# Optimization experiments

Measured on AMD Instinct MI355X. Metric: run time of the kernel, lower is better.

Reference implementation:

```python
import jax, jax.numpy as jnp
import numpy as np
import math

B = 16          # graphs per batch
N = 2048        # nodes per graph
F_IN = 64       # input node features
E_PER = 32768   # edges per graph
E = B * E_PER
H = 128         # hidden width (fixed by module)
C = 10          # output classes
K = math.ceil(0.8 * N)  # TopKPooling keep count per graph = 1639


def setup_inputs() -> dict:
    key = jax.random.key(0)
    ks = jax.random.split(key, 24)
    x = jax.random.normal(ks[0], (B * N, F_IN), jnp.float32)
    # intra-graph random edges (source->target), global node ids
    gid = jnp.repeat(jnp.arange(B, dtype=jnp.int32), E_PER)
    src = gid * N + jax.random.randint(ks[1], (E,), 0, N, dtype=jnp.int32)
    dst = gid * N + jax.random.randint(ks[2], (E,), 0, N, dtype=jnp.int32)

    def lin_w(k, o, i):
        return jax.random.normal(k, (o, i), jnp.float32) / jnp.sqrt(i)

    inp = dict(x=x, src=src, dst=dst)
    # GraphConv: lin_rel (with bias) on aggregated neighbors + lin_root (no bias)
    inp.update(W1_rel=lin_w(ks[3], H, F_IN), b1=jnp.zeros((H,), jnp.float32), W1_root=lin_w(ks[4], H, F_IN))
    inp.update(W2_rel=lin_w(ks[5], H, H), b2=jnp.zeros((H,), jnp.float32), W2_root=lin_w(ks[6], H, H))
    inp.update(W3_rel=lin_w(ks[7], H, H), b3=jnp.zeros((H,), jnp.float32), W3_root=lin_w(ks[8], H, H))
    inp.update(pool_w=jax.random.normal(ks[9], (H,), jnp.float32) / jnp.sqrt(H))
    inp.update(Wl1=lin_w(ks[10], 128, 256), bl1=jnp.zeros((128,), jnp.float32))
    inp.update(Wl2=lin_w(ks[11], 64, 128), bl2=jnp.zeros((64,), jnp.float32))
    inp.update(Wl3=lin_w(ks[12], C, 64), bl3=jnp.zeros((C,), jnp.float32))
    return inp


def _graph_conv(x, src, dst, W_rel, b, W_root, n_nodes, emask=None):
    # out_i = W_rel @ (sum_{j->i} x_j) + b + W_root @ x_i
    msg = x[src]
    if emask is not None:
        msg = msg * emask[:, None]
    agg = jax.ops.segment_sum(msg, dst, num_segments=n_nodes)
    return agg @ W_rel.T + b + x @ W_root.T


def _global_pools(x, n_per_graph):
    xb = x.reshape(B, n_per_graph, -1)
    return jnp.concatenate([xb.max(axis=1), xb.mean(axis=1)], axis=1)  # [B, 2F]


def reference(x, src, dst, W1_rel, b1, W1_root, W2_rel, b2, W2_root,
              W3_rel, b3, W3_root, pool_w, Wl1, bl1, Wl2, bl2, Wl3, bl3):
    n0 = B * N
    h = jax.nn.relu(_graph_conv(x, src, dst, W1_rel, b1, W1_root, n0))
    x1 = _global_pools(h, N)

    h = jax.nn.relu(_graph_conv(h, src, dst, W2_rel, b2, W2_root, n0))

    # TopKPooling(ratio=0.8): score = tanh(x@w/||w||); keep top-k per graph;
    # kept features scaled by score; edges with a dropped endpoint removed.
    score = jnp.tanh((h @ pool_w) / jnp.linalg.norm(pool_w))  # [B*N]
    top_s, top_i = jax.lax.top_k(score.reshape(B, N), K)      # [B,K]
    perm = (top_i + jnp.arange(B)[:, None] * N).reshape(-1)   # global old ids [B*K]
    h = h[perm] * top_s.reshape(-1)[:, None]                  # [B*K, H]

    n1 = B * K
    new_id = jnp.full((n0,), -1, jnp.int32).at[perm].set(jnp.arange(n1, dtype=jnp.int32))
    ns, nd = new_id[src], new_id[dst]
    keep = ((ns >= 0) & (nd >= 0)).astype(h.dtype)
    ns = jnp.where(ns >= 0, ns, 0)
    nd = jnp.where(nd >= 0, nd, 0)

    x2 = _global_pools(h, K)
    h = jax.nn.relu(_graph_conv(h, ns, nd, W3_rel, b3, W3_root, n1, emask=keep))
    x3 = _global_pools(h, K)

    z = x1 + x2 + x3
    z = jax.nn.relu(z @ Wl1.T + bl1)
    z = jax.nn.relu(z @ Wl2.T + bl2)
    return jax.nn.log_softmax(z @ Wl3.T + bl3, axis=-1)  # [B, C]
```

## Files before the change

### kernel.cpp

```cpp
#include <hip/hip_runtime.h>
#include <hip/hip_bf16.h>
#include <math.h>

#define NB 32768
#define NN 2048
#define BG 16
#define KK 1639
#define KKP 1664
#define N1 (BG*KK)
#define N1P (BG*KKP)
#define EE 524288
#define HH 128
#define FIN 64

using half8 = __attribute__((ext_vector_type(8))) _Float16;
using half4 = __attribute__((ext_vector_type(4))) _Float16;
using f32x4 = __attribute__((ext_vector_type(4))) float;

__device__ __forceinline__ void acc4(f32x4& a, const float4& v) {
  a[0] += v.x; a[1] += v.y; a[2] += v.z; a[3] += v.w;
}

__global__ void deg_kernel(const int* __restrict__ dst, int* deg, int n) {
  int e = blockIdx.x * blockDim.x + threadIdx.x;
  if (e < n) atomicAdd(&deg[dst[e]], 1);
}

__global__ void exscan_kernel(const int* __restrict__ deg, int* rs, int* cursor, int n) {
  __shared__ int wsum[16];
  __shared__ int carry;
  int t = threadIdx.x;
  int lane = t & 63, wid = t >> 6;
  if (t == 0) carry = 0;
  __syncthreads();
  int ntiles = (n + 4095) >> 12;
  for (int tile = 0; tile < ntiles; ++tile) {
    int idx = (tile << 12) + t * 4;
    int4 v4 = *(const int4*)(deg + idx);
    int v0 = (idx + 0 < n) ? v4.x : 0;
    int v1 = (idx + 1 < n) ? v4.y : 0;
    int v2 = (idx + 2 < n) ? v4.z : 0;
    int v3 = (idx + 3 < n) ? v4.w : 0;
    int s = v0 + v1 + v2 + v3;
    int pre = s;
#pragma unroll
    for (int off = 1; off < 64; off <<= 1) {
      int u = __shfl_up(pre, off, 64);
      if (lane >= off) pre += u;
    }
    if (lane == 63) wsum[wid] = pre;
    __syncthreads();
    int wbase = 0;
#pragma unroll
    for (int ww = 0; ww < 16; ++ww)
      if (ww < wid) wbase += wsum[ww];
    int ex = carry + wbase + (pre - s);
    int4 e4 = make_int4(ex, ex + v0, ex + v0 + v1, ex + v0 + v1 + v2);
    if (idx + 3 < n) {
      *(int4*)(rs + idx) = e4;
      *(int4*)(cursor + idx) = e4;
    } else {
      if (idx + 0 < n) { rs[idx + 0] = e4.x; cursor[idx + 0] = e4.x; }
      if (idx + 1 < n) { rs[idx + 1] = e4.y; cursor[idx + 1] = e4.y; }
      if (idx + 2 < n) { rs[idx + 2] = e4.z; cursor[idx + 2] = e4.z; }
    }
    int tot = 0;
    if (t == 1023) tot = ex + s;
    __syncthreads();
    if (t == 1023) carry = tot;
    __syncthreads();
  }
  if (t == 0) rs[n] = carry;
}

__global__ void scatter_kernel(const int* __restrict__ src, const int* __restrict__ dst,
                               int* cursor, int* csr, int n) {
  int e = blockIdx.x * blockDim.x + threadIdx.x;
  if (e < n) {
    int d = dst[e];
    int p = atomicAdd(&cursor[d], 1);
    csr[p] = src[e];
  }
}

template <int KD1, int KD2, int POOL, int SCORE, int REMAP>
__global__ __launch_bounds__(512, 4) void conv_mfma(
    const float* __restrict__ feat, const float* __restrict__ xr,
    const int* __restrict__ rs, const int* __restrict__ csr,
    const int* __restrict__ perm, const int* __restrict__ new_id,
    const _Float16* __restrict__ Wh, const _Float16* __restrict__ Wl,
    const float* __restrict__ bias, float* __restrict__ out, int M, int nwg,
    float* __restrict__ pmax, float* __restrict__ psum,
    const float* __restrict__ pw, float* __restrict__ score) {
  constexpr int KTOT = KD1 + KD2;
  constexpr int NSTEP = KTOT / 32;
  __shared__ _Float16 ah_lds[64 * KTOT];
  __shared__ _Float16 al_lds[64 * KTOT];
  __shared__ float sdot[64][8];
  __shared__ float swsq[8];

  int tid = threadIdx.x;
  int lane = tid & 63, wid = tid >> 6;
  int bq = nwg >> 3, br = nwg & 7, bx = blockIdx.x & 7, bi = blockIdx.x >> 3;
  int swz = (bx < br ? bx * (bq + 1) : br * (bq + 1) + (bx - br) * bq) + bi;
  int row0 = swz * 64;
  int ch0 = wid * 16;
  int col = lane & 15;
  int kseg = (lane >> 4) * 8;

  {
    constexpr int CH = KD1 / 4;
    constexpr int EPW = 64 / CH;
    int sub = lane / CH;
    int ch = lane % CH;
    const float4* feat4 = (const float4*)feat;
#pragma unroll
    for (int rr = 0; rr < 8; ++rr) {
      int gr = wid * 8 + rr;
      int grow = row0 + gr;
      int e0 = 0, e1 = 0;
      if (REMAP) {
        int g = grow / KKP, j = grow - g * KKP;
        if (j < KK) {
          int oldrow = perm[g * KK + j];
          e0 = rs[oldrow];
          e1 = rs[oldrow + 1];
        }
      } else {
        if (grow >= M) grow = M - 1;
        e0 = rs[grow];
        e1 = rs[grow + 1];
      }
      f32x4 a0 = {0.f, 0.f, 0.f, 0.f}, a1 = a0, a2 = a0, a3 = a0;
      int e = e0 + sub;
      for (; e + 7 * EPW < e1; e += 8 * EPW) {
        int c[8];
#pragma unroll
        for (int u = 0; u < 8; ++u) c[u] = csr[e + u * EPW];
        if (REMAP) {
#pragma unroll
          for (int u = 0; u < 8; ++u) c[u] = new_id[c[u]];
        }
        float4 v[8];
#pragma unroll
        for (int u = 0; u < 8; ++u) {
          int ci = (REMAP && c[u] < 0) ? 0 : c[u];
          v[u] = feat4[(size_t)ci * CH + ch];
        }
        if (REMAP) {
#pragma unroll
          for (int u = 0; u < 8; ++u)
            if (c[u] < 0) v[u] = make_float4(0.f, 0.f, 0.f, 0.f);
        }
        acc4(a0, v[0]); acc4(a1, v[1]); acc4(a2, v[2]); acc4(a3, v[3]);
        acc4(a0, v[4]); acc4(a1, v[5]); acc4(a2, v[6]); acc4(a3, v[7]);
      }
      for (; e + 3 * EPW < e1; e += 4 * EPW) {
        int c[4];
#pragma unroll
        for (int u = 0; u < 4; ++u) c[u] = csr[e + u * EPW];
        if (REMAP) {
#pragma unroll
          for (int u = 0; u < 4; ++u) c[u] = new_id[c[u]];
        }
        float4 v[4];
#pragma unroll
        for (int u = 0; u < 4; ++u) {
          int ci = (REMAP && c[u] < 0) ? 0 : c[u];
          v[u] = feat4[(size_t)ci * CH + ch];
        }
        if (REMAP) {
#pragma unroll
          for (int u = 0; u < 4; ++u)
            if (c[u] < 0) v[u] = make_float4(0.f, 0.f, 0.f, 0.f);
        }
        acc4(a0, v[0]); acc4(a1, v[1]); acc4(a2, v[2]); acc4(a3, v[3]);
      }
      for (; e < e1; e += EPW) {
        int c = csr[e];
        if (REMAP) {
          c = new_id[c];
          if (c < 0) continue;
        }
        float4 v = feat4[(size_t)c * CH + ch];
        acc4(a0, v);
      }
      f32x4 s = (a0 + a1) + (a2 + a3);
      if (EPW == 4) {
#pragma unroll
        for (int j = 0; j < 4; ++j) s[j] += __shfl_xor(s[j], 16, 64);
      }
#pragma unroll
      for (int j = 0; j < 4; ++j) s[j] += __shfl_xor(s[j], 32, 64);
      if (sub == 0) {
        half4 hi, lo;
#pragma unroll
        for (int j = 0; j < 4; ++j) {
          _Float16 h = (_Float16)s[j];
          hi[j] = h;
          lo[j] = (_Float16)(s[j] - (float)h);
        }
        int byte = ((gr * KTOT + ch * 4) * 2) ^ ((gr & 7) << 4);
        *(half4*)((char*)ah_lds + byte) = hi;
        *(half4*)((char*)al_lds + byte) = lo;
      }
    }
  }

  for (int idx = tid; idx < 64 * KD2 / 8; idx += 512) {
    int row = idx / (KD2 / 8);
    int kc = (idx % (KD2 / 8)) * 8;
    int grow = row0 + row;
    if (grow >= M) grow = M - 1;
    const float* sp = xr + (size_t)grow * KD2 + kc;
    float4 a0 = *(const float4*)sp;
    float4 a1 = *(const float4*)(sp + 4);
    float av[8] = {a0.x, a0.y, a0.z, a0.w, a1.x, a1.y, a1.z, a1.w};
    half8 vh, vl;
#pragma unroll
    for (int j = 0; j < 8; ++j) {
      _Float16 h = (_Float16)av[j];
      vh[j] = h;
      vl[j] = (_Float16)(av[j] - (float)h);
    }
    int byte = ((row * KTOT + KD1 + kc) * 2) ^ ((row & 7) << 4);
    *(half8*)((char*)ah_lds + byte) = vh;
    *(half8*)((char*)al_lds + byte) = vl;
  }

  size_t wbase = (size_t)(ch0 + col) * KTOT + kseg;
  half8 whc = *(const half8*)(Wh + wbase);
  half8 wlc = *(const half8*)(Wl + wbase);
  __syncthreads();

  f32x4 acc[4];
#pragma unroll
  for (int rf = 0; rf < 4; ++rf) acc[rf] = (f32x4){0.f, 0.f, 0.f, 0.f};
  int r = lane & 15;
#pragma unroll
  for (int s = 0; s < NSTEP; ++s) {
    half8 whn, wln;
    if (s + 1 < NSTEP) {
      whn = *(const half8*)(Wh + wbase + (s + 1) * 32);
      wln = *(const half8*)(Wl + wbase + (s + 1) * 32);
    }
#pragma unroll
    for (int rf = 0; rf < 4; ++rf) {
      int row = rf * 16 + r;
      int byte = ((row * KTOT + s * 32 + kseg) * 2) ^ ((row & 7) << 4);
      half8 a_h = *(const half8*)((const char*)ah_lds + byte);
      half8 a_l = *(const half8*)((const char*)al_lds + byte);
      acc[rf] = __builtin_amdgcn_mfma_f32_16x16x32_f16(a_l, whc, acc[rf], 0, 0, 0);
      acc[rf] = __builtin_amdgcn_mfma_f32_16x16x32_f16(a_h, wlc, acc[rf], 0, 0, 0);
      acc[rf] = __builtin_amdgcn_mfma_f32_16x16x32_f16(a_h, whc, acc[rf], 0, 0, 0);
    }
    if (s + 1 < NSTEP) { whc = whn; wlc = wln; }
  }

  float bv = bias[ch0 + col];
  float cmax = -3.402823466e38f, csum = 0.f;
  float wcol = SCORE ? pw[ch0 + col] : 0.f;
  float pd[4][4];
  int g = 0, rowbase = 0;
  if (POOL == 2) { g = row0 / KKP; rowbase = row0 - g * KKP; }
#pragma unroll
  for (int rf = 0; rf < 4; ++rf) {
    int orow0 = row0 + rf * 16 + (lane >> 4) * 4;
#pragma unroll
    for (int rr = 0; rr < 4; ++rr) {
      int orow = orow0 + rr;
      float v = fmaxf(acc[rf][rr] + bv, 0.f);
      if (orow < M) out[(size_t)orow * HH + ch0 + col] = v;
      if (POOL == 1) { cmax = fmaxf(cmax, v); csum += v; }
      if (POOL == 2) {
        int local = rowbase + rf * 16 + (lane >> 4) * 4 + rr;
        if (local < KK) { cmax = fmaxf(cmax, v); csum += v; }
      }
      if (SCORE) pd[rf][rr] = v * wcol;
    }
  }
  if (POOL) {
    cmax = fmaxf(cmax, __shfl_xor(cmax, 16, 64)); csum += __shfl_xor(csum, 16, 64);
    cmax = fmaxf(cmax, __shfl_xor(cmax, 32, 64)); csum += __shfl_xor(csum, 32, 64);
    if ((lane >> 4) == 0) {
      if (POOL == 1) {
        int gg = row0 >> 11, sb = (row0 & 2047) >> 6;
        pmax[(gg * 32 + sb) * HH + ch0 + col] = cmax;
        psum[(gg * 32 + sb) * HH + ch0 + col] = csum;
      } else {
        int sb = rowbase >> 6;
        pmax[(g * 26 + sb) * HH + ch0 + col] = cmax;
        psum[(g * 26 + sb) * HH + ch0 + col] = csum;
      }
    }
  }
  if (SCORE) {
#pragma unroll
    for (int rf = 0; rf < 4; ++rf)
#pragma unroll
      for (int rr = 0; rr < 4; ++rr) {
        float d = pd[rf][rr];
        d += __shfl_xor(d, 1, 64); d += __shfl_xor(d, 2, 64);
        d += __shfl_xor(d, 4, 64); d += __shfl_xor(d, 8, 64);
        if (col == 0) sdot[rf * 16 + (lane >> 4) * 4 + rr][wid] = d;
      }
    float wsq = wcol * wcol;
    wsq += __shfl_xor(wsq, 1, 64); wsq += __shfl_xor(wsq, 2, 64);
    wsq += __shfl_xor(wsq, 4, 64); wsq += __shfl_xor(wsq, 8, 64);
    if (lane == 0) swsq[wid] = wsq;
    __syncthreads();
    if (tid < 64) {
      float d = 0.f, q = 0.f;
#pragma unroll
      for (int wv = 0; wv < 8; ++wv) { d += sdot[tid][wv]; q += swsq[wv]; }
      score[row0 + tid] = tanhf(d * rsqrtf(q));
    }
  }
}

__global__ void prep_weights_f16(const float* __restrict__ W1_rel, const float* __restrict__ W1_root,
                                 const float* __restrict__ W2_rel, const float* __restrict__ W2_root,
                                 const float* __restrict__ W3_rel, const float* __restrict__ W3_root,
                                 _Float16* wh1, _Float16* wl1, _Float16* wh2, _Float16* wl2,
                                 _Float16* wh3, _Float16* wl3) {
  int idx = blockIdx.x * blockDim.x + threadIdx.x;
  float v;
  _Float16* ph;
  _Float16* pl;
  int j;
  if (idx < 128 * 128) {
    j = idx;
    int o = j >> 7, k = j & 127;
    v = (k < 64) ? W1_rel[o * 64 + k] : W1_root[o * 64 + (k - 64)];
    ph = wh1; pl = wl1;
  } else if (idx < 128 * 128 + 128 * 256) {
    j = idx - 128 * 128;
    int o = j >> 8, k = j & 255;
    v = (k < 128) ? W2_rel[o * 128 + k] : W2_root[o * 128 + (k - 128)];
    ph = wh2; pl = wl2;
  } else if (idx < 128 * 128 + 2 * 128 * 256) {
    j = idx - 128 * 128 - 128 * 256;
    int o = j >> 8, k = j & 255;
    v = (k < 128) ? W3_rel[o * 128 + k] : W3_root[o * 128 + (k - 128)];
    ph = wh3; pl = wl3;
  } else {
    return;
  }
  _Float16 h = (_Float16)v;
  ph[j] = h;
  pl[j] = (_Float16)(v - (float)h);
}

__global__ void topk_kernel(const float* __restrict__ score, int* perm) {
  __shared__ unsigned long long keys[NN];
  __shared__ int hist[256];
  __shared__ unsigned long long sP;
  __shared__ int srem;
  __shared__ int scnt;
  int b = blockIdx.x, t = threadIdx.x;
  for (int i = t; i < NN; i += 256) {
    float s = score[b * NN + i];
    unsigned u = __float_as_uint(s);
    u = (u & 0x80000000u) ? ~u : (u | 0x80000000u);
    keys[i] = ((unsigned long long)u << 32) | (unsigned)(NN - 1 - i);
  }
  if (t == 0) { sP = 0ULL; srem = KK; scnt = 0; }
  __syncthreads();
  for (int pass = 0; pass < 8; ++pass) {
    int shift = 56 - 8 * pass;
    for (int i = t; i < 256; i += 256) hist[i] = 0;
    __syncthreads();
    unsigned long long P = sP;
    unsigned long long hm = (pass == 0) ? 0ULL : (~0ULL) << (shift + 8);
    for (int i = t; i < NN; i += 256) {
      unsigned long long k = keys[i];
      if (((k ^ P) & hm) == 0) atomicAdd(&hist[(int)((k >> shift) & 255)], 1);
    }
    __syncthreads();
    if (t < 64) {
      int l = t;
      int c[4], part = 0;
#pragma unroll
      for (int q = 0; q < 4; ++q) { c[q] = hist[255 - (l * 4 + q)]; part += c[q]; }
      int pre = part;
#pragma unroll
      for (int off = 1; off < 64; off <<= 1) {
        int u2 = __shfl_up(pre, off, 64);
        if (l >= off) pre += u2;
      }
      int excl = pre - part;
      int rem = srem;
      if (excl < rem && rem <= excl + part) {
        int run = excl;
#pragma unroll
        for (int q = 0; q < 4; ++q) {
          if (run + c[q] >= rem) {
            srem = rem - run;
            sP = sP | ((unsigned long long)(255 - (l * 4 + q)) << shift);
            break;
          }
          run += c[q];
        }
      }
    }
    __syncthreads();
  }
  unsigned long long T = sP;
  for (int i = t; i < NN; i += 256) {
    if (keys[i] >= T) {
      int pos = atomicAdd(&scnt, 1);
      perm[b * KK + pos] = b * NN + (NN - 1 - (int)(keys[i] & 0xffffffffULL));
    }
  }
}

__global__ void h3_kernel(const float4* __restrict__ h2, const int* __restrict__ perm,
                          const float* __restrict__ score, float4* __restrict__ h3,
                          int* __restrict__ new_id) {
  int idx = blockIdx.x * blockDim.x + threadIdx.x;
  if (idx < N1 * 32) {
    int g = idx >> 5, c = idx & 31;
    int b = g / KK, j = g - b * KK;
    int p = perm[g];
    if (c == 0) new_id[p] = b * KKP + j;
    float s = score[p];
    float4 v = h2[(size_t)p * 32 + c];
    v.x *= s; v.y *= s; v.z *= s; v.w *= s;
    h3[(size_t)(b * KKP + j) * 32 + c] = v;
  }
}

__global__ void pool2_kernel(const float* __restrict__ h, float* pmax, float* psum) {
  int b = blockIdx.x / 26, s = blockIdx.x % 26;
  int f = threadIdx.x;
  int r0 = s * 64, r1 = min(KK, r0 + 64);
  float m = -3.402823466e38f, sum = 0.f;
  for (int r = r0; r < r1; ++r) {
    float v = h[(size_t)(b * KKP + r) * HH + f];
    m = fmaxf(m, v);
    sum += v;
  }
  pmax[(b * 26 + s) * HH + f] = m;
  psum[(b * 26 + s) * HH + f] = sum;
}

__global__ void mlp_kernel(const float* __restrict__ pm1, const float* __restrict__ ps1,
                           const float* __restrict__ pm2, const float* __restrict__ ps2,
                           const float* __restrict__ pm3, const float* __restrict__ ps3,
                           const float* __restrict__ Wl1, const float* __restrict__ bl1,
                           const float* __restrict__ Wl2, const float* __restrict__ bl2,
                           const float* __restrict__ Wl3, const float* __restrict__ bl3,
                           float* out) {
  __shared__ float z[256], a1[128], a2[64], a3[10], red[2];
  int b = blockIdx.x, t = threadIdx.x;
  float m1 = -3.402823466e38f, m2 = m1, m3 = m1;
  float s1 = 0.f, s2 = 0.f, s3 = 0.f;
  for (int s = 0; s < 32; ++s) {
    int o = (b * 32 + s) * 128 + t;
    m1 = fmaxf(m1, pm1[o]); s1 += ps1[o];
  }
  for (int s = 0; s < 26; ++s) {
    int o = (b * 26 + s) * 128 + t;
    m2 = fmaxf(m2, pm2[o]); s2 += ps2[o];
    m3 = fmaxf(m3, pm3[o]); s3 += ps3[o];
  }
  z[t] = m1 + m2 + m3;
  z[128 + t] = s1 * (1.f / NN) + (s2 + s3) * (1.f / KK);
  __syncthreads();
  {
    float acc = bl1[t];
    for (int q = 0; q < 256; ++q) acc = fmaf(Wl1[t * 256 + q], z[q], acc);
    a1[t] = fmaxf(acc, 0.f);
  }
  __syncthreads();
  if (t < 64) {
    float acc = bl2[t];
    for (int q = 0; q < 128; ++q) acc = fmaf(Wl2[t * 128 + q], a1[q], acc);
    a2[t] = fmaxf(acc, 0.f);
  }
  __syncthreads();
  if (t < 10) {
    float acc = bl3[t];
    for (int q = 0; q < 64; ++q) acc = fmaf(Wl3[t * 64 + q], a2[q], acc);
    a3[t] = acc;
  }
  __syncthreads();
  if (t == 0) {
    float m = a3[0];
    for (int i = 1; i < 10; ++i) m = fmaxf(m, a3[i]);
    float s = 0.f;
    for (int i = 0; i < 10; ++i) s += expf(a3[i] - m);
    red[0] = m;
    red[1] = logf(s);
  }
  __syncthreads();
  if (t < 10) out[b * 10 + t] = a3[t] - red[0] - red[1];
}

extern "C" void kernel_launch(void* const* d_in, const int* in_sizes, int n_in,
                              void* d_out, int out_size, void* d_ws, size_t ws_size,
                              hipStream_t stream) {
  const float* x       = (const float*)d_in[0];
  const int*   src     = (const int*)d_in[1];
  const int*   dst     = (const int*)d_in[2];
  const float* W1_rel  = (const float*)d_in[3];
  const float* b1      = (const float*)d_in[4];
  const float* W1_root = (const float*)d_in[5];
  const float* W2_rel  = (const float*)d_in[6];
  const float* b2      = (const float*)d_in[7];
  const float* W2_root = (const float*)d_in[8];
  const float* W3_rel  = (const float*)d_in[9];
  const float* b3      = (const float*)d_in[10];
  const float* W3_root = (const float*)d_in[11];
  const float* pool_w  = (const float*)d_in[12];
  const float* Wl1     = (const float*)d_in[13];
  const float* bl1     = (const float*)d_in[14];
  const float* Wl2     = (const float*)d_in[15];
  const float* bl2     = (const float*)d_in[16];
  const float* Wl3     = (const float*)d_in[17];
  const float* bl3     = (const float*)d_in[18];
  float* out = (float*)d_out;

  char* w = (char*)d_ws;
  size_t off = 0;
  auto alloc = [&](size_t bytes) -> char* {
    off = (off + 255) & ~(size_t)255;
    char* p = w + off;
    off += bytes;
    return p;
  };
  int* deg1     = (int*)alloc((NB + 4096) * 4);
  int* rs1      = (int*)alloc((NB + 1) * 4);
  int* cursor1  = (int*)alloc(NB * 4);
  int* csr1     = (int*)alloc((size_t)EE * 4);
  int* new_id   = (int*)alloc(NB * 4);
  int* perm     = (int*)alloc(N1 * 4);
  _Float16* wh1 = (_Float16*)alloc(128 * 128 * 2);
  _Float16* wl1 = (_Float16*)alloc(128 * 128 * 2);
  _Float16* wh2 = (_Float16*)alloc(128 * 256 * 2);
  _Float16* wl2 = (_Float16*)alloc(128 * 256 * 2);
  _Float16* wh3 = (_Float16*)alloc(128 * 256 * 2);
  _Float16* wl3 = (_Float16*)alloc(128 * 256 * 2);
  float* bufA   = (float*)alloc((size_t)NB * HH * 4);
  float* bufB   = (float*)alloc((size_t)NB * HH * 4);
  float* score  = (float*)alloc(NB * 4);
  float* pm1    = (float*)alloc(BG * 32 * HH * 4);
  float* ps1    = (float*)alloc(BG * 32 * HH * 4);
  float* pm2    = (float*)alloc(BG * 26 * HH * 4);
  float* ps2    = (float*)alloc(BG * 26 * HH * 4);
  float* pm3    = (float*)alloc(BG * 26 * HH * 4);
  float* ps3    = (float*)alloc(BG * 26 * HH * 4);
  if (off > ws_size) return;

  const int TB = 256;
  const int egrid = (EE + TB - 1) / TB;

  hipMemsetAsync(deg1, 0, (NB + 4096) * 4, stream);
  hipMemsetAsync(new_id, 0xFF, NB * 4, stream);

  prep_weights_f16<<<(128 * 128 + 2 * 128 * 256 + TB - 1) / TB, TB, 0, stream>>>(
      W1_rel, W1_root, W2_rel, W2_root, W3_rel, W3_root, wh1, wl1, wh2, wl2, wh3, wl3);

  deg_kernel<<<egrid, TB, 0, stream>>>(dst, deg1, EE);
  exscan_kernel<<<1, 1024, 0, stream>>>(deg1, rs1, cursor1, NB);
  scatter_kernel<<<egrid, TB, 0, stream>>>(src, dst, cursor1, csr1, EE);

  conv_mfma<64, 64, 1, 0, 0><<<NB / 64, 512, 0, stream>>>(
      x, x, rs1, csr1, nullptr, nullptr, wh1, wl1, b1, bufA, NB, NB / 64, pm1, ps1,
      nullptr, nullptr);

  conv_mfma<128, 128, 0, 1, 0><<<NB / 64, 512, 0, stream>>>(
      bufA, bufA, rs1, csr1, nullptr, nullptr, wh2, wl2, b2, bufB, NB, NB / 64,
      nullptr, nullptr, pool_w, score);

  topk_kernel<<<BG, 256, 0, stream>>>(score, perm);
  h3_kernel<<<(N1 * 32 + TB - 1) / TB, TB, 0, stream>>>((const float4*)bufB, perm, score,
                                                        (float4*)bufA, new_id);
  pool2_kernel<<<BG * 26, 128, 0, stream>>>(bufA, pm2, ps2);

  conv_mfma<128, 128, 2, 0, 1><<<N1P / 64, 512, 0, stream>>>(
      bufA, bufA, rs1, csr1, perm, new_id, wh3, wl3, b3, bufB, N1P, N1P / 64, pm3, ps3,
      nullptr, nullptr);

  mlp_kernel<<<BG, 128, 0, stream>>>(pm1, ps1, pm2, ps2, pm3, ps3,
                                     Wl1, bl1, Wl2, bl2, Wl3, bl3, out);
}
```

Baseline: 227.5 us.

## Precompute remapped CSR and row ranges for pooled conv; fold memsets into prep

Adds a remap pass that writes a new-id-translated copy of the CSR column array, and has h3_kernel record per-new-row edge start/end offsets. The third conv then reads those directly instead of doing a dependent new_id lookup per edge and a perm/rs indirection per row. The two hipMemsetAsync calls are folded into the weight-prep kernel. This costs an extra full pass over the edge list and extra workspace for csr3.

```diff
diff --git a/kernel.cpp b/kernel.cpp
--- a/kernel.cpp
+++ b/kernel.cpp
@@ -83,11 +83,17 @@
   }
 }
 
+__global__ void remap_kernel(const int* __restrict__ csr1, const int* __restrict__ new_id,
+                             int* __restrict__ csr3, int n) {
+  int e = blockIdx.x * blockDim.x + threadIdx.x;
+  if (e < n) csr3[e] = new_id[csr1[e]];
+}
+
 template <int KD1, int KD2, int POOL, int SCORE, int REMAP>
 __global__ __launch_bounds__(512, 4) void conv_mfma(
     const float* __restrict__ feat, const float* __restrict__ xr,
     const int* __restrict__ rs, const int* __restrict__ csr,
-    const int* __restrict__ perm, const int* __restrict__ new_id,
+    const int* __restrict__ rows3, const int* __restrict__ rowe3,
     const _Float16* __restrict__ Wh, const _Float16* __restrict__ Wl,
     const float* __restrict__ bias, float* __restrict__ out, int M, int nwg,
     float* __restrict__ pmax, float* __restrict__ psum,
@@ -118,14 +124,10 @@
     for (int rr = 0; rr < 8; ++rr) {
       int gr = wid * 8 + rr;
       int grow = row0 + gr;
-      int e0 = 0, e1 = 0;
+      int e0, e1;
       if (REMAP) {
-        int g = grow / KKP, j = grow - g * KKP;
-        if (j < KK) {
-          int oldrow = perm[g * KK + j];
-          e0 = rs[oldrow];
-          e1 = rs[oldrow + 1];
-        }
+        e0 = rows3[grow];
+        e1 = rowe3[grow];
       } else {
         if (grow >= M) grow = M - 1;
         e0 = rs[grow];
@@ -137,10 +139,6 @@
         int c[8];
 #pragma unroll
         for (int u = 0; u < 8; ++u) c[u] = csr[e + u * EPW];
-        if (REMAP) {
-#pragma unroll
-          for (int u = 0; u < 8; ++u) c[u] = new_id[c[u]];
-        }
         float4 v[8];
 #pragma unroll
         for (int u = 0; u < 8; ++u) {
@@ -159,10 +157,6 @@
         int c[4];
 #pragma unroll
         for (int u = 0; u < 4; ++u) c[u] = csr[e + u * EPW];
-        if (REMAP) {
-#pragma unroll
-          for (int u = 0; u < 4; ++u) c[u] = new_id[c[u]];
-        }
         float4 v[4];
 #pragma unroll
         for (int u = 0; u < 4; ++u) {
@@ -178,10 +172,7 @@
       }
       for (; e < e1; e += EPW) {
         int c = csr[e];
-        if (REMAP) {
-          c = new_id[c];
-          if (c < 0) continue;
-        }
+        if (REMAP && c < 0) continue;
         float4 v = feat4[(size_t)c * CH + ch];
         acc4(a0, v);
       }
@@ -318,12 +309,17 @@
   }
 }
 
-__global__ void prep_weights_f16(const float* __restrict__ W1_rel, const float* __restrict__ W1_root,
-                                 const float* __restrict__ W2_rel, const float* __restrict__ W2_root,
-                                 const float* __restrict__ W3_rel, const float* __restrict__ W3_root,
-                                 _Float16* wh1, _Float16* wl1, _Float16* wh2, _Float16* wl2,
-                                 _Float16* wh3, _Float16* wl3) {
+__global__ void prep_kernel(const float* __restrict__ W1_rel, const float* __restrict__ W1_root,
+                            const float* __restrict__ W2_rel, const float* __restrict__ W2_root,
+                            const float* __restrict__ W3_rel, const float* __restrict__ W3_root,
+                            _Float16* wh1, _Float16* wl1, _Float16* wh2, _Float16* wl2,
+                            _Float16* wh3, _Float16* wl3,
+                            int* __restrict__ deg1, int* __restrict__ new_id,
+                            int* __restrict__ rows3, int* __restrict__ rowe3) {
   int idx = blockIdx.x * blockDim.x + threadIdx.x;
+  if (idx < NB + 4096) deg1[idx] = 0;
+  if (idx < NB) new_id[idx] = -1;
+  if (idx < N1P) { rows3[idx] = 0; rowe3[idx] = 0; }
   float v;
   _Float16* ph;
   _Float16* pl;
@@ -415,18 +411,24 @@
 }
 
 __global__ void h3_kernel(const float4* __restrict__ h2, const int* __restrict__ perm,
-                          const float* __restrict__ score, float4* __restrict__ h3,
-                          int* __restrict__ new_id) {
+                          const float* __restrict__ score, const int* __restrict__ rs1,
+                          float4* __restrict__ h3, int* __restrict__ new_id,
+                          int* __restrict__ rows3, int* __restrict__ rowe3) {
   int idx = blockIdx.x * blockDim.x + threadIdx.x;
   if (idx < N1 * 32) {
     int g = idx >> 5, c = idx & 31;
     int b = g / KK, j = g - b * KK;
     int p = perm[g];
-    if (c == 0) new_id[p] = b * KKP + j;
+    int pj = b * KKP + j;
+    if (c == 0) {
+      new_id[p] = pj;
+      rows3[pj] = rs1[p];
+      rowe3[pj] = rs1[p + 1];
+    }
     float s = score[p];
     float4 v = h2[(size_t)p * 32 + c];
     v.x *= s; v.y *= s; v.z *= s; v.w *= s;
-    h3[(size_t)(b * KKP + j) * 32 + c] = v;
+    h3[(size_t)pj * 32 + c] = v;
   }
 }
 
@@ -533,8 +535,11 @@
   int* rs1      = (int*)alloc((NB + 1) * 4);
   int* cursor1  = (int*)alloc(NB * 4);
   int* csr1     = (int*)alloc((size_t)EE * 4);
+  int* csr3     = (int*)alloc((size_t)EE * 4);
   int* new_id   = (int*)alloc(NB * 4);
   int* perm     = (int*)alloc(N1 * 4);
+  int* rows3    = (int*)alloc(N1P * 4);
+  int* rowe3    = (int*)alloc(N1P * 4);
   _Float16* wh1 = (_Float16*)alloc(128 * 128 * 2);
   _Float16* wl1 = (_Float16*)alloc(128 * 128 * 2);
   _Float16* wh2 = (_Float16*)alloc(128 * 256 * 2);
@@ -555,11 +560,9 @@
   const int TB = 256;
   const int egrid = (EE + TB - 1) / TB;
 
-  hipMemsetAsync(deg1, 0, (NB + 4096) * 4, stream);
-  hipMemsetAsync(new_id, 0xFF, NB * 4, stream);
-
-  prep_weights_f16<<<(128 * 128 + 2 * 128 * 256 + TB - 1) / TB, TB, 0, stream>>>(
-      W1_rel, W1_root, W2_rel, W2_root, W3_rel, W3_root, wh1, wl1, wh2, wl2, wh3, wl3);
+  prep_kernel<<<(128 * 128 + 2 * 128 * 256 + TB - 1) / TB, TB, 0, stream>>>(
+      W1_rel, W1_root, W2_rel, W2_root, W3_rel, W3_root, wh1, wl1, wh2, wl2, wh3, wl3,
+      deg1, new_id, rows3, rowe3);
 
   deg_kernel<<<egrid, TB, 0, stream>>>(dst, deg1, EE);
   exscan_kernel<<<1, 1024, 0, stream>>>(deg1, rs1, cursor1, NB);
@@ -575,11 +578,13 @@
 
   topk_kernel<<<BG, 256, 0, stream>>>(score, perm);
   h3_kernel<<<(N1 * 32 + TB - 1) / TB, TB, 0, stream>>>((const float4*)bufB, perm, score,
-                                                        (float4*)bufA, new_id);
+                                                        rs1, (float4*)bufA, new_id,
+                                                        rows3, rowe3);
+  remap_kernel<<<egrid, TB, 0, stream>>>(csr1, new_id, csr3, EE);
   pool2_kernel<<<BG * 26, 128, 0, stream>>>(bufA, pm2, ps2);
 
-  conv_mfma<128, 128, 2, 0, 1><<<N1P / 64, 512, 0, stream>>>(
-      bufA, bufA, rs1, csr1, perm, new_id, wh3, wl3, b3, bufB, N1P, N1P / 64, pm3, ps3,
+  conv_mfma<128, 128, 2, 0, 2><<<N1P / 64, 512, 0, stream>>>(
+      bufA, bufA, nullptr, csr3, rows3, rowe3, wh3, wl3, b3, bufB, N1P, N1P / 64, pm3, ps3,
       nullptr, nullptr);
 
   mlp_kernel<<<BG, 128, 0, stream>>>(pm1, ps1, pm2, ps2, pm3, ps3,
```

Result: faster. 220.5 us (-3.1%).
